# Kernel optimization log

Hardware: AMD Instinct MI355X
Metric: run time of the kernel (lower is better)

Reference implementation:

```python
import jax, jax.numpy as jnp
import numpy as np

B, C, L, H = 4, 512, 2048, 8
D = C // H  # head_dim


def setup_inputs() -> dict:
    key = jax.random.key(0)
    ks = jax.random.split(key, 9)
    s = 1.0 / np.sqrt(C)  # keep logits well-scaled like torch Linear init
    return {
        "x": jax.random.normal(ks[0], (B, C, L), dtype=jnp.float32),
        "Wq": jax.random.normal(ks[1], (C, C), dtype=jnp.float32) * s,
        "bq": jnp.zeros((C,), dtype=jnp.float32),
        "Wk": jax.random.normal(ks[2], (C, C), dtype=jnp.float32) * s,
        "bk": jnp.zeros((C,), dtype=jnp.float32),
        "Wv": jax.random.normal(ks[3], (C, C), dtype=jnp.float32) * s,
        "bv": jnp.zeros((C,), dtype=jnp.float32),
        "Wo": jax.random.normal(ks[4], (C, C), dtype=jnp.float32) * s,
        "bo": jnp.zeros((C,), dtype=jnp.float32),
    }


def reference(x, Wq, bq, Wk, bk, Wv, bv, Wo, bo):
    # x: (B, C, L) -> (B, L, C)
    xp = jnp.transpose(x, (0, 2, 1))
    scale = D ** (-0.5)

    def heads(w, b):
        y = xp @ w.T + b                      # (B, L, C)  torch Linear: x W^T + b
        return y.reshape(B, L, H, D).transpose(0, 2, 1, 3)  # (B, H, L, D)

    q = heads(Wq, bq)
    k = heads(Wk, bk)
    v = heads(Wv, bv)

    attn = jnp.einsum('bhqd,bhkd->bhqk', q, k) * scale  # (B, H, L, L)
    attn = jax.nn.softmax(attn, axis=-1)
    out = jnp.einsum('bhqk,bhkd->bhqd', attn, v)        # (B, H, L, D)
    out = out.transpose(0, 2, 1, 3).reshape(B, L, C)    # (B, L, C)
    out = out @ Wo.T + bo
    return x + jnp.transpose(out, (0, 2, 1))            # residual in (B, C, L)
```

## Files before the change

### kernel.cpp

```cpp
#include <hip/hip_runtime.h>
#include <math.h>

#define B_ 4
#define C_ 512
#define L_ 2048
#define H_ 8
#define D_ 64
#define QSCALE 0.18033688011112042f
#define DEFER_THR 12.0f

typedef __bf16 bf16x8 __attribute__((ext_vector_type(8)));
typedef float f32x4 __attribute__((ext_vector_type(4)));

__device__ __forceinline__ unsigned cvt_pk(float lo, float hi) {
    unsigned r;
    asm("v_cvt_pk_bf16_f32 %0, %1, %2" : "=v"(r) : "v"(lo), "v"(hi));
    return r;
}
__device__ __forceinline__ unsigned short f2bf_hw(float a) {
    unsigned r;
    asm("v_cvt_pk_bf16_f32 %0, %1, %1" : "=v"(r) : "v"(a));
    return (unsigned short)r;
}
__device__ __forceinline__ bf16x8 frag_ld(const unsigned short* p) {
    uint4 v = *reinterpret_cast<const uint4*>(p);
    return __builtin_bit_cast(bf16x8, v);
}
__device__ __forceinline__ float fmax3(float a, float b, float c) {
    return fmaxf(fmaxf(a, b), c);
}
__device__ __forceinline__ void glds16(const void* g, void* l) {
    __builtin_amdgcn_global_load_lds(
        (const __attribute__((address_space(1))) void*)g,
        (__attribute__((address_space(3))) void*)l, 16, 0, 0);
}

__global__ __launch_bounds__(256) void prep(
    const float* __restrict__ x,
    const float* __restrict__ w0, const float* __restrict__ w1,
    const float* __restrict__ w2, const float* __restrict__ w3,
    unsigned short* __restrict__ xt,
    unsigned short* __restrict__ o0, unsigned short* __restrict__ o1,
    unsigned short* __restrict__ o2, unsigned short* __restrict__ o3)
{
    __shared__ float T[64][68];
    const int t = threadIdx.x;

    if (blockIdx.z < B_) {
        const int b  = blockIdx.z;
        const int l0 = blockIdx.x * 64;
        const int c0 = blockIdx.y * 64;
        const float* xb = x + (size_t)b * C_ * L_;
        unsigned short* xtb = xt + (size_t)b * L_ * C_;

        #pragma unroll
        for (int p = 0; p < 4; ++p) {
            const int ci = 16 * p + (t >> 4);
            const int l4 = (t & 15) * 4;
            *reinterpret_cast<float4*>(&T[ci][l4]) =
                *reinterpret_cast<const float4*>(xb + (size_t)(c0 + ci) * L_ + l0 + l4);
        }
        __syncthreads();

        const int lo = t >> 2;
        const int cb = (t & 3) * 16;
        unsigned w[8];
        #pragma unroll
        for (int k = 0; k < 8; ++k)
            w[k] = cvt_pk(T[cb + 2 * k][lo], T[cb + 2 * k + 1][lo]);
        unsigned short* dst = xtb + (size_t)(l0 + lo) * C_ + c0 + cb;
        *reinterpret_cast<uint4*>(dst)     = make_uint4(w[0], w[1], w[2], w[3]);
        *reinterpret_cast<uint4*>(dst + 8) = make_uint4(w[4], w[5], w[6], w[7]);
    } else {
        const int m = blockIdx.z - B_;
        const float* src; unsigned short* dst;
        if      (m == 0) { src = w0; dst = o0; }
        else if (m == 1) { src = w1; dst = o1; }
        else if (m == 2) { src = w2; dst = o2; }
        else             { src = w3; dst = o3; }
        const int flat = blockIdx.x + 32 * blockIdx.y;
        const size_t idx = ((size_t)flat * 256 + t) * 4;
        const float4 v = *reinterpret_cast<const float4*>(src + idx);
        *reinterpret_cast<uint2*>(dst + idx) =
            make_uint2(cvt_pk(v.x, v.y), cvt_pk(v.z, v.w));
    }
}

__global__ __launch_bounds__(256) void qkv_gemm(
    const unsigned short* __restrict__ xt,
    const unsigned short* __restrict__ wq, const unsigned short* __restrict__ wk,
    const unsigned short* __restrict__ wv,
    const float* __restrict__ bq, const float* __restrict__ bk,
    const float* __restrict__ bv,
    unsigned short* __restrict__ qb, unsigned short* __restrict__ kb,
    unsigned short* __restrict__ vb)
{
    __shared__ unsigned short As[2][128][32];
    __shared__ unsigned short Bs[2][128][32];

    const int mode = blockIdx.z >> 2;
    const int b    = blockIdx.z & 3;
    const size_t LC = (size_t)L_ * C_;

    const unsigned short *A, *Bt;
    const float* bias;
    unsigned short* Out;
    float scale = 1.0f;
    int m0, n0, oN, biasN;
    if (mode == 0) {
        A = xt + (size_t)b * LC; Bt = wq; bias = bq; Out = qb + (size_t)b * LC;
        m0 = blockIdx.y * 128; n0 = blockIdx.x * 128; oN = C_; biasN = 1;
        scale = QSCALE;
    } else if (mode == 1) {
        A = xt + (size_t)b * LC; Bt = wk; bias = bk; Out = kb + (size_t)b * LC;
        m0 = blockIdx.y * 128; n0 = blockIdx.x * 128; oN = C_; biasN = 1;
    } else {
        A = wv; Bt = xt + (size_t)b * LC; bias = bv; Out = vb + (size_t)b * LC;
        m0 = blockIdx.x * 128; n0 = blockIdx.y * 128; oN = L_; biasN = 0;
    }
    const int doswz = (mode != 0);

    const int t = threadIdx.x;
    const int lane = t & 63, wid = t >> 6;
    const int wm = (wid >> 1) * 64, wn = (wid & 1) * 64;
    const int q16 = lane & 15, g = lane >> 4;

    const int gr = wid * 32 + (lane >> 2);
    const int gc = (lane & 3) * 8;
    const unsigned short* Ap0 = A  + (size_t)(m0 + gr) * C_ + gc;
    const unsigned short* Ap1 = Ap0 + 16 * C_;
    const unsigned short* Bp0 = Bt + (size_t)(n0 + gr) * C_ + gc;
    const unsigned short* Bp1 = Bp0 + 16 * C_;

    f32x4 zero4 = {0.f, 0.f, 0.f, 0.f};
    f32x4 acc[4][4];
    #pragma unroll
    for (int i = 0; i < 4; ++i)
        #pragma unroll
        for (int j = 0; j < 4; ++j) acc[i][j] = zero4;

    glds16(Ap0, &As[0][wid * 32][0]);      glds16(Ap1, &As[0][wid * 32 + 16][0]);
    glds16(Bp0, &Bs[0][wid * 32][0]);      glds16(Bp1, &Bs[0][wid * 32 + 16][0]);
    __syncthreads();

    #pragma unroll 2
    for (int it = 0; it < 16; ++it) {
        const int cur = it & 1;
        if (it < 15) {
            const int ko = (it + 1) * 32;
            glds16(Ap0 + ko, &As[cur ^ 1][wid * 32][0]);
            glds16(Ap1 + ko, &As[cur ^ 1][wid * 32 + 16][0]);
            glds16(Bp0 + ko, &Bs[cur ^ 1][wid * 32][0]);
            glds16(Bp1 + ko, &Bs[cur ^ 1][wid * 32 + 16][0]);
        }
        bf16x8 af[4], bfr[4];
        #pragma unroll
        for (int i = 0; i < 4; ++i) af[i]  = frag_ld(&As[cur][wm + 16 * i + q16][8 * g]);
        #pragma unroll
        for (int j = 0; j < 4; ++j) bfr[j] = frag_ld(&Bs[cur][wn + 16 * j + q16][8 * g]);
        #pragma unroll
        for (int i = 0; i < 4; ++i)
            #pragma unroll
            for (int j = 0; j < 4; ++j)
                acc[i][j] = __builtin_amdgcn_mfma_f32_16x16x32_bf16(
                    af[i], bfr[j], acc[i][j], 0, 0, 0);
        __syncthreads();
    }

    #pragma unroll
    for (int j = 0; j < 4; ++j) {
        const int n = n0 + wn + 16 * j + q16;
        const float bn = biasN ? bias[n] : 0.f;
        #pragma unroll
        for (int i = 0; i < 4; ++i) {
            #pragma unroll
            for (int r = 0; r < 4; ++r) {
                const int m = m0 + wm + 16 * i + 4 * g + r;
                const float v = acc[i][j][r] + (biasN ? bn : bias[m]);
                const int nn = doswz ? (n ^ ((m & 7) << 3)) : n;
                Out[(size_t)m * oN + nn] = f2bf_hw(v * scale);
            }
        }
    }
}

__global__ __launch_bounds__(256) void gemm_out(
    const unsigned short* __restrict__ A,
    const unsigned short* __restrict__ Bt,
    const float* __restrict__ bias,
    float* __restrict__ Out, const float* __restrict__ resid)
{
    __shared__ unsigned short As[128][40];
    __shared__ unsigned short Bs[128][40];

    const int bz = blockIdx.z;
    const size_t LC = (size_t)L_ * C_;
    Bt    += (size_t)bz * LC;
    Out   += (size_t)bz * LC;
    resid += (size_t)bz * LC;

    const int n0 = blockIdx.x * 128;
    const int m0 = blockIdx.y * 128;
    const int t  = threadIdx.x;
    const int lane = t & 63, wid = t >> 6;
    const int wm = (wid >> 1) * 64, wn = (wid & 1) * 64;
    const int q16 = lane & 15, g = lane >> 4;

    const int srow = t >> 1;
    const int scol = (t & 1) * 16;
    const unsigned short* Ap = A  + (size_t)(m0 + srow) * C_ + scol;
    const unsigned short* Bp = Bt + (size_t)(n0 + srow) * C_ + scol;

    f32x4 zero4 = {0.f, 0.f, 0.f, 0.f};
    f32x4 acc[4][4];
    #pragma unroll
    for (int i = 0; i < 4; ++i)
        #pragma unroll
        for (int j = 0; j < 4; ++j) acc[i][j] = zero4;

    uint4 ar0 = *reinterpret_cast<const uint4*>(Ap);
    uint4 ar1 = *reinterpret_cast<const uint4*>(Ap + 8);
    uint4 br0 = *reinterpret_cast<const uint4*>(Bp);
    uint4 br1 = *reinterpret_cast<const uint4*>(Bp + 8);

    for (int k0 = 0; k0 < C_; k0 += 32) {
        __syncthreads();
        *reinterpret_cast<uint4*>(&As[srow][scol])     = ar0;
        *reinterpret_cast<uint4*>(&As[srow][scol + 8]) = ar1;
        *reinterpret_cast<uint4*>(&Bs[srow][scol])     = br0;
        *reinterpret_cast<uint4*>(&Bs[srow][scol + 8]) = br1;
        __syncthreads();
        if (k0 + 32 < C_) {
            ar0 = *reinterpret_cast<const uint4*>(Ap + k0 + 32);
            ar1 = *reinterpret_cast<const uint4*>(Ap + k0 + 40);
            br0 = *reinterpret_cast<const uint4*>(Bp + k0 + 32);
            br1 = *reinterpret_cast<const uint4*>(Bp + k0 + 40);
        }
        bf16x8 af[4], bfr[4];
        #pragma unroll
        for (int i = 0; i < 4; ++i) af[i]  = frag_ld(&As[wm + 16 * i + q16][8 * g]);
        #pragma unroll
        for (int j = 0; j < 4; ++j) bfr[j] = frag_ld(&Bs[wn + 16 * j + q16][8 * g]);
        #pragma unroll
        for (int i = 0; i < 4; ++i)
            #pragma unroll
            for (int j = 0; j < 4; ++j)
                acc[i][j] = __builtin_amdgcn_mfma_f32_16x16x32_bf16(
                    af[i], bfr[j], acc[i][j], 0, 0, 0);
    }

    #pragma unroll
    for (int j = 0; j < 4; ++j) {
        const int n = n0 + wn + 16 * j + q16;
        #pragma unroll
        for (int i = 0; i < 4; ++i) {
            #pragma unroll
            for (int r = 0; r < 4; ++r) {
                const int m = m0 + wm + 16 * i + 4 * g + r;
                const size_t off = (size_t)m * L_ + n;
                Out[off] = acc[i][j][r] + bias[m] + resid[off];
            }
        }
    }
}

__global__ __launch_bounds__(256) void attn_mfma(
    const unsigned short* __restrict__ Qb,
    const unsigned short* __restrict__ Kb,
    const unsigned short* __restrict__ Vb,
    unsigned short* __restrict__ Ab)
{
    __shared__ unsigned short Ks[2][64][64];
    __shared__ unsigned short Vs[2][64][64];
    __shared__ unsigned short Pw[4][16][64];

    const int q0 = blockIdx.x * 64;
    const int h  = blockIdx.y;
    const int b  = blockIdx.z;
    const int t  = threadIdx.x, lane = t & 63, wid = t >> 6;
    const int q16 = lane & 15, g = lane >> 4;
    const int swz = (q16 & 7) << 3;
    const int h4  = (q16 & 7) << 2;

    const unsigned short* Qg = Qb + (size_t)b * L_ * C_;
    const unsigned short* Kg = Kb + (size_t)b * L_ * C_ + h * D_;
    const unsigned short* Vg = Vb + ((size_t)b * C_ + h * D_) * L_;
    unsigned short* Ag       = Ab + (size_t)b * L_ * C_;

    unsigned* pw = reinterpret_cast<unsigned*>(&Pw[wid][q16][0]);

    bf16x8 qf[2];
    {
        const unsigned short* qp =
            Qg + (size_t)(q0 + 16 * wid + q16) * C_ + h * D_ + 8 * g;
        qf[0] = frag_ld(qp);
        qf[1] = frag_ld(qp + 32);
    }

    const unsigned ow = (q16 == 0) ? 0x3F803F80u : 0u;
    const uint4 ov = make_uint4(ow, ow, ow, ow);
    const bf16x8 onesf = __builtin_bit_cast(bf16x8, ov);

    f32x4 zero4 = {0.f, 0.f, 0.f, 0.f};
    f32x4 oacc[4], lacc = zero4;
    #pragma unroll
    for (int n = 0; n < 4; ++n) oacc[n] = zero4;
    float m_s = -INFINITY;

    const int gr8 = lane >> 3;
    const int gc8 = (lane & 7) * 8;
    const unsigned short* Kp0 = Kg + (size_t)(16 * wid     + gr8) * C_ + gc8;
    const unsigned short* Kp1 = Kg + (size_t)(16 * wid + 8 + gr8) * C_ + gc8;
    const unsigned short* Vp0 = Vg + (size_t)(16 * wid     + gr8) * L_ + gc8;
    const unsigned short* Vp1 = Vg + (size_t)(16 * wid + 8 + gr8) * L_ + gc8;

    glds16(Kp0, &Ks[0][16 * wid][0]);
    glds16(Kp1, &Ks[0][16 * wid + 8][0]);
    glds16(Vp0, &Vs[0][16 * wid][0]);
    glds16(Vp1, &Vs[0][16 * wid + 8][0]);
    __syncthreads();

    #pragma unroll 2
    for (int kt = 0; kt < 32; ++kt) {
        const int cur = kt & 1;
        if (kt < 31) {
            const size_t ko = (size_t)(kt + 1) * 64;
            glds16(Kp0 + ko * C_, &Ks[cur ^ 1][16 * wid][0]);
            glds16(Kp1 + ko * C_, &Ks[cur ^ 1][16 * wid + 8][0]);
            glds16(Vp0 + ko,      &Vs[cur ^ 1][16 * wid][0]);
            glds16(Vp1 + ko,      &Vs[cur ^ 1][16 * wid + 8][0]);
        }

        f32x4 sacc[4];
        #pragma unroll
        for (int f = 0; f < 4; ++f) sacc[f] = zero4;
        #pragma unroll
        for (int s = 0; s < 2; ++s) {
            #pragma unroll
            for (int f = 0; f < 4; ++f) {
                bf16x8 kf = frag_ld(&Ks[cur][16 * f + q16][(32 * s + 8 * g) ^ swz]);
                sacc[f] = __builtin_amdgcn_mfma_f32_16x16x32_bf16(
                    kf, qf[s], sacc[f], 0, 0, 0);
            }
        }

        const float t0 = fmax3(sacc[0][0], sacc[0][1], sacc[0][2]);
        const float t1 = fmax3(sacc[0][3], sacc[1][0], sacc[1][1]);
        const float t2 = fmax3(sacc[1][2], sacc[1][3], sacc[2][0]);
        const float t3 = fmax3(sacc[2][1], sacc[2][2], sacc[2][3]);
        const float t4 = fmax3(sacc[3][0], sacc[3][1], sacc[3][2]);
        float pm = fmaxf(fmax3(t0, t1, t2), fmax3(t3, t4, sacc[3][3]));
        pm = fmaxf(pm, __shfl_xor(pm, 16));
        pm = fmaxf(pm, __shfl_xor(pm, 32));

        if (!__all(pm - m_s <= DEFER_THR)) {
            const float mn   = fmaxf(m_s, pm);
            const float corr = exp2f(m_s - mn);
            m_s = mn;
            #pragma unroll
            for (int r = 0; r < 4; ++r) {
                const float c_o = __shfl(corr, 20 * g + r);
                #pragma unroll
                for (int n = 0; n < 4; ++n) oacc[n][r] *= c_o;
                lacc[r] *= c_o;
            }
        }

        float p[4][4];
        #pragma unroll
        for (int f = 0; f < 4; ++f)
            #pragma unroll
            for (int r = 0; r < 4; ++r) p[f][r] = exp2f(sacc[f][r] - m_s);

        #pragma unroll
        for (int f = 0; f < 4; ++f) {
            uint2 v2;
            v2.x = cvt_pk(p[f][0], p[f][1]);
            v2.y = cvt_pk(p[f][2], p[f][3]);
            *reinterpret_cast<uint2*>(pw + ((8 * f + 2 * g) ^ h4)) = v2;
        }

        #pragma unroll
        for (int s2 = 0; s2 < 2; ++s2) {
            bf16x8 pf = frag_ld(reinterpret_cast<const unsigned short*>(
                pw + ((16 * s2 + 4 * g) ^ h4)));
            #pragma unroll
            for (int n = 0; n < 4; ++n) {
                bf16x8 vf = frag_ld(&Vs[cur][16 * n + q16][(32 * s2 + 8 * g) ^ swz]);
                oacc[n] = __builtin_amdgcn_mfma_f32_16x16x32_bf16(
                    pf, vf, oacc[n], 0, 0, 0);
            }
            lacc = __builtin_amdgcn_mfma_f32_16x16x32_bf16(
                pf, onesf, lacc, 0, 0, 0);
        }

        __syncthreads();
    }

    #pragma unroll
    for (int r = 0; r < 4; ++r) {
        const float l_o = __shfl(lacc[r], lane & 48);
        const float inv = 1.f / l_o;
        const int q = q0 + 16 * wid + 4 * g + r;
        #pragma unroll
        for (int n = 0; n < 4; ++n)
            Ag[(size_t)q * C_ + h * D_ + 16 * n + q16] = f2bf_hw(oacc[n][r] * inv);
    }
}

extern "C" void kernel_launch(void* const* d_in, const int* in_sizes, int n_in,
                              void* d_out, int out_size, void* d_ws, size_t ws_size,
                              hipStream_t stream)
{
    const float* x  = (const float*)d_in[0];
    const float* Wq = (const float*)d_in[1];
    const float* bq = (const float*)d_in[2];
    const float* Wk = (const float*)d_in[3];
    const float* bk = (const float*)d_in[4];
    const float* Wv = (const float*)d_in[5];
    const float* bv = (const float*)d_in[6];
    const float* Wo = (const float*)d_in[7];
    const float* bo = (const float*)d_in[8];
    float* out = (float*)d_out;

    const size_t NB = (size_t)B_ * L_ * C_;
    const size_t NW = (size_t)C_ * C_;
    unsigned short* ws16 = (unsigned short*)d_ws;
    unsigned short* xt  = ws16;
    unsigned short* qb  = xt  + NB;
    unsigned short* kb  = qb  + NB;
    unsigned short* vb  = kb  + NB;
    unsigned short* att = vb  + NB;
    unsigned short* wqb = att + NB;
    unsigned short* wkb = wqb + NW;
    unsigned short* wvb = wkb + NW;
    unsigned short* wob = wvb + NW;

    prep<<<dim3(32, 8, 2 * B_), 256, 0, stream>>>(
        x, Wq, Wk, Wv, Wo, xt, wqb, wkb, wvb, wob);

    qkv_gemm<<<dim3(4, 16, 3 * B_), 256, 0, stream>>>(
        xt, wqb, wkb, wvb, bq, bk, bv, qb, kb, vb);

    attn_mfma<<<dim3(L_ / 64, H_, B_), 256, 0, stream>>>(qb, kb, vb, att);

    gemm_out<<<dim3(16, 4, B_), 256, 0, stream>>>(wob, att, bo, out, x);
}
```

Baseline: 225.1 us.

## Use 32x32 MFMA attention with register P via permlane swap; async double-buffer out GEMM

The attention kernel now uses 32x32x16 MFMA tiles with 128 queries per block, so each block reuses each K/V tile across twice as many queries. It also keeps P in registers, repacking it with v_permlane32_swap instead of round-tripping through LDS. The output GEMM now loads tiles with global-to-LDS direct loads into double-buffered shared memory, replacing register staging and dropping one of the two syncs per k-step. The trade-offs are fewer blocks (512 attention blocks), higher register pressure from the 16-wide accumulators, and unpadded LDS rows in the GEMM that may cause bank conflicts.

```diff
diff --git a/kernel.cpp b/kernel.cpp
--- a/kernel.cpp
+++ b/kernel.cpp
@@ -11,6 +11,7 @@
 
 typedef __bf16 bf16x8 __attribute__((ext_vector_type(8)));
 typedef float f32x4 __attribute__((ext_vector_type(4)));
+typedef float f32x16 __attribute__((ext_vector_type(16)));
 
 __device__ __forceinline__ unsigned cvt_pk(float lo, float hi) {
     unsigned r;
@@ -190,8 +191,8 @@
     const float* __restrict__ bias,
     float* __restrict__ Out, const float* __restrict__ resid)
 {
-    __shared__ unsigned short As[128][40];
-    __shared__ unsigned short Bs[128][40];
+    __shared__ unsigned short As[2][128][32];
+    __shared__ unsigned short Bs[2][128][32];
 
     const int bz = blockIdx.z;
     const size_t LC = (size_t)L_ * C_;
@@ -206,10 +207,12 @@
     const int wm = (wid >> 1) * 64, wn = (wid & 1) * 64;
     const int q16 = lane & 15, g = lane >> 4;
 
-    const int srow = t >> 1;
-    const int scol = (t & 1) * 16;
-    const unsigned short* Ap = A  + (size_t)(m0 + srow) * C_ + scol;
-    const unsigned short* Bp = Bt + (size_t)(n0 + srow) * C_ + scol;
+    const int gr = wid * 32 + (lane >> 2);
+    const int gc = (lane & 3) * 8;
+    const unsigned short* Ap0 = A  + (size_t)(m0 + gr) * C_ + gc;
+    const unsigned short* Ap1 = Ap0 + 16 * C_;
+    const unsigned short* Bp0 = Bt + (size_t)(n0 + gr) * C_ + gc;
+    const unsigned short* Bp1 = Bp0 + 16 * C_;
 
     f32x4 zero4 = {0.f, 0.f, 0.f, 0.f};
     f32x4 acc[4][4];
@@ -218,35 +221,32 @@
         #pragma unroll
         for (int j = 0; j < 4; ++j) acc[i][j] = zero4;
 
-    uint4 ar0 = *reinterpret_cast<const uint4*>(Ap);
-    uint4 ar1 = *reinterpret_cast<const uint4*>(Ap + 8);
-    uint4 br0 = *reinterpret_cast<const uint4*>(Bp);
-    uint4 br1 = *reinterpret_cast<const uint4*>(Bp + 8);
-
-    for (int k0 = 0; k0 < C_; k0 += 32) {
-        __syncthreads();
-        *reinterpret_cast<uint4*>(&As[srow][scol])     = ar0;
-        *reinterpret_cast<uint4*>(&As[srow][scol + 8]) = ar1;
-        *reinterpret_cast<uint4*>(&Bs[srow][scol])     = br0;
-        *reinterpret_cast<uint4*>(&Bs[srow][scol + 8]) = br1;
-        __syncthreads();
-        if (k0 + 32 < C_) {
-            ar0 = *reinterpret_cast<const uint4*>(Ap + k0 + 32);
-            ar1 = *reinterpret_cast<const uint4*>(Ap + k0 + 40);
-            br0 = *reinterpret_cast<const uint4*>(Bp + k0 + 32);
-            br1 = *reinterpret_cast<const uint4*>(Bp + k0 + 40);
+    glds16(Ap0, &As[0][wid * 32][0]);      glds16(Ap1, &As[0][wid * 32 + 16][0]);
+    glds16(Bp0, &Bs[0][wid * 32][0]);      glds16(Bp1, &Bs[0][wid * 32 + 16][0]);
+    __syncthreads();
+
+    #pragma unroll 2
+    for (int it = 0; it < 16; ++it) {
+        const int cur = it & 1;
+        if (it < 15) {
+            const int ko = (it + 1) * 32;
+            glds16(Ap0 + ko, &As[cur ^ 1][wid * 32][0]);
+            glds16(Ap1 + ko, &As[cur ^ 1][wid * 32 + 16][0]);
+            glds16(Bp0 + ko, &Bs[cur ^ 1][wid * 32][0]);
+            glds16(Bp1 + ko, &Bs[cur ^ 1][wid * 32 + 16][0]);
         }
         bf16x8 af[4], bfr[4];
         #pragma unroll
-        for (int i = 0; i < 4; ++i) af[i]  = frag_ld(&As[wm + 16 * i + q16][8 * g]);
-        #pragma unroll
-        for (int j = 0; j < 4; ++j) bfr[j] = frag_ld(&Bs[wn + 16 * j + q16][8 * g]);
+        for (int i = 0; i < 4; ++i) af[i]  = frag_ld(&As[cur][wm + 16 * i + q16][8 * g]);
+        #pragma unroll
+        for (int j = 0; j < 4; ++j) bfr[j] = frag_ld(&Bs[cur][wn + 16 * j + q16][8 * g]);
         #pragma unroll
         for (int i = 0; i < 4; ++i)
             #pragma unroll
             for (int j = 0; j < 4; ++j)
                 acc[i][j] = __builtin_amdgcn_mfma_f32_16x16x32_bf16(
                     af[i], bfr[j], acc[i][j], 0, 0, 0);
+        __syncthreads();
     }
 
     #pragma unroll
@@ -272,47 +272,42 @@
 {
     __shared__ unsigned short Ks[2][64][64];
     __shared__ unsigned short Vs[2][64][64];
-    __shared__ unsigned short Pw[4][16][64];
-
-    const int q0 = blockIdx.x * 64;
+
+    const int q0 = blockIdx.x * 128;
     const int h  = blockIdx.y;
     const int b  = blockIdx.z;
     const int t  = threadIdx.x, lane = t & 63, wid = t >> 6;
-    const int q16 = lane & 15, g = lane >> 4;
-    const int swz = (q16 & 7) << 3;
-    const int h4  = (q16 & 7) << 2;
+    const int q32 = lane & 31, hi = lane >> 5;
+    const int swz = (q32 & 7) << 3;
 
     const unsigned short* Qg = Qb + (size_t)b * L_ * C_;
     const unsigned short* Kg = Kb + (size_t)b * L_ * C_ + h * D_;
     const unsigned short* Vg = Vb + ((size_t)b * C_ + h * D_) * L_;
     unsigned short* Ag       = Ab + (size_t)b * L_ * C_;
 
-    unsigned* pw = reinterpret_cast<unsigned*>(&Pw[wid][q16][0]);
-
-    bf16x8 qf[2];
+    bf16x8 qf[4];
     {
         const unsigned short* qp =
-            Qg + (size_t)(q0 + 16 * wid + q16) * C_ + h * D_ + 8 * g;
-        qf[0] = frag_ld(qp);
-        qf[1] = frag_ld(qp + 32);
-    }
-
-    const unsigned ow = (q16 == 0) ? 0x3F803F80u : 0u;
+            Qg + (size_t)(q0 + 32 * wid + q32) * C_ + h * D_ + 8 * hi;
+        #pragma unroll
+        for (int c = 0; c < 4; ++c) qf[c] = frag_ld(qp + 16 * c);
+    }
+
+    const unsigned ow = (q32 == 0) ? 0x3F803F80u : 0u;
     const uint4 ov = make_uint4(ow, ow, ow, ow);
     const bf16x8 onesf = __builtin_bit_cast(bf16x8, ov);
 
-    f32x4 zero4 = {0.f, 0.f, 0.f, 0.f};
-    f32x4 oacc[4], lacc = zero4;
-    #pragma unroll
-    for (int n = 0; n < 4; ++n) oacc[n] = zero4;
+    f32x16 zero16 = {0.f,0.f,0.f,0.f,0.f,0.f,0.f,0.f,
+                     0.f,0.f,0.f,0.f,0.f,0.f,0.f,0.f};
+    f32x16 oacc0 = zero16, oacc1 = zero16, lacc = zero16;
     float m_s = -INFINITY;
 
     const int gr8 = lane >> 3;
     const int gc8 = (lane & 7) * 8;
-    const unsigned short* Kp0 = Kg + (size_t)(16 * wid     + gr8) * C_ + gc8;
-    const unsigned short* Kp1 = Kg + (size_t)(16 * wid + 8 + gr8) * C_ + gc8;
-    const unsigned short* Vp0 = Vg + (size_t)(16 * wid     + gr8) * L_ + gc8;
-    const unsigned short* Vp1 = Vg + (size_t)(16 * wid + 8 + gr8) * L_ + gc8;
+    const unsigned short* Kp0 = Kg + (size_t)(16 * wid + gr8) * C_ + gc8;
+    const unsigned short* Kp1 = Kp0 + (size_t)8 * C_;
+    const unsigned short* Vp0 = Vg + (size_t)(16 * wid + gr8) * L_ + gc8;
+    const unsigned short* Vp1 = Vp0 + (size_t)8 * L_;
 
     glds16(Kp0, &Ks[0][16 * wid][0]);
     glds16(Kp1, &Ks[0][16 * wid + 8][0]);
@@ -331,26 +326,31 @@
             glds16(Vp1 + ko,      &Vs[cur ^ 1][16 * wid + 8][0]);
         }
 
-        f32x4 sacc[4];
-        #pragma unroll
-        for (int f = 0; f < 4; ++f) sacc[f] = zero4;
-        #pragma unroll
-        for (int s = 0; s < 2; ++s) {
-            #pragma unroll
-            for (int f = 0; f < 4; ++f) {
-                bf16x8 kf = frag_ld(&Ks[cur][16 * f + q16][(32 * s + 8 * g) ^ swz]);
-                sacc[f] = __builtin_amdgcn_mfma_f32_16x16x32_bf16(
-                    kf, qf[s], sacc[f], 0, 0, 0);
-            }
-        }
-
-        const float t0 = fmax3(sacc[0][0], sacc[0][1], sacc[0][2]);
-        const float t1 = fmax3(sacc[0][3], sacc[1][0], sacc[1][1]);
-        const float t2 = fmax3(sacc[1][2], sacc[1][3], sacc[2][0]);
-        const float t3 = fmax3(sacc[2][1], sacc[2][2], sacc[2][3]);
-        const float t4 = fmax3(sacc[3][0], sacc[3][1], sacc[3][2]);
-        float pm = fmaxf(fmax3(t0, t1, t2), fmax3(t3, t4, sacc[3][3]));
-        pm = fmaxf(pm, __shfl_xor(pm, 16));
+        f32x16 s0 = zero16, s1 = zero16;
+        #pragma unroll
+        for (int c = 0; c < 4; ++c) {
+            const int co = (16 * c + 8 * hi) ^ swz;
+            bf16x8 k0 = frag_ld(&Ks[cur][q32][co]);
+            bf16x8 k1 = frag_ld(&Ks[cur][32 + q32][co]);
+            s0 = __builtin_amdgcn_mfma_f32_32x32x16_bf16(k0, qf[c], s0, 0, 0, 0);
+            s1 = __builtin_amdgcn_mfma_f32_32x32x16_bf16(k1, qf[c], s1, 0, 0, 0);
+        }
+
+        const float a0 = fmax3(s0[0], s0[1], s0[2]);
+        const float a1 = fmax3(s0[3], s0[4], s0[5]);
+        const float a2 = fmax3(s0[6], s0[7], s0[8]);
+        const float a3 = fmax3(s0[9], s0[10], s0[11]);
+        const float a4 = fmax3(s0[12], s0[13], s0[14]);
+        const float a5 = fmax3(s0[15], s1[0], s1[1]);
+        const float a6 = fmax3(s1[2], s1[3], s1[4]);
+        const float a7 = fmax3(s1[5], s1[6], s1[7]);
+        const float a8 = fmax3(s1[8], s1[9], s1[10]);
+        const float a9 = fmax3(s1[11], s1[12], s1[13]);
+        const float b0 = fmax3(a0, a1, a2);
+        const float b1 = fmax3(a3, a4, a5);
+        const float b2 = fmax3(a6, a7, a8);
+        const float b3 = fmax3(a9, s1[14], s1[15]);
+        float pm = fmaxf(fmaxf(b0, b1), fmaxf(b2, b3));
         pm = fmaxf(pm, __shfl_xor(pm, 32));
 
         if (!__all(pm - m_s <= DEFER_THR)) {
@@ -358,53 +358,52 @@
             const float corr = exp2f(m_s - mn);
             m_s = mn;
             #pragma unroll
-            for (int r = 0; r < 4; ++r) {
-                const float c_o = __shfl(corr, 20 * g + r);
-                #pragma unroll
-                for (int n = 0; n < 4; ++n) oacc[n][r] *= c_o;
-                lacc[r] *= c_o;
+            for (int r = 0; r < 16; ++r) {
+                const float cr = __shfl(corr, (r & 3) + 8 * (r >> 2) + 4 * hi);
+                oacc0[r] *= cr; oacc1[r] *= cr; lacc[r] *= cr;
             }
         }
 
-        float p[4][4];
-        #pragma unroll
-        for (int f = 0; f < 4; ++f)
-            #pragma unroll
-            for (int r = 0; r < 4; ++r) p[f][r] = exp2f(sacc[f][r] - m_s);
-
-        #pragma unroll
-        for (int f = 0; f < 4; ++f) {
-            uint2 v2;
-            v2.x = cvt_pk(p[f][0], p[f][1]);
-            v2.y = cvt_pk(p[f][2], p[f][3]);
-            *reinterpret_cast<uint2*>(pw + ((8 * f + 2 * g) ^ h4)) = v2;
-        }
-
-        #pragma unroll
-        for (int s2 = 0; s2 < 2; ++s2) {
-            bf16x8 pf = frag_ld(reinterpret_cast<const unsigned short*>(
-                pw + ((16 * s2 + 4 * g) ^ h4)));
-            #pragma unroll
-            for (int n = 0; n < 4; ++n) {
-                bf16x8 vf = frag_ld(&Vs[cur][16 * n + q16][(32 * s2 + 8 * g) ^ swz]);
-                oacc[n] = __builtin_amdgcn_mfma_f32_16x16x32_bf16(
-                    pf, vf, oacc[n], 0, 0, 0);
-            }
-            lacc = __builtin_amdgcn_mfma_f32_16x16x32_bf16(
-                pf, onesf, lacc, 0, 0, 0);
+        float p0[16], p1[16];
+        #pragma unroll
+        for (int r = 0; r < 16; ++r) {
+            p0[r] = exp2f(s0[r] - m_s);
+            p1[r] = exp2f(s1[r] - m_s);
+        }
+
+        #pragma unroll
+        for (int ks = 0; ks < 4; ++ks) {
+            const int rb = 8 * (ks & 1);
+            #define PPX(i) ((ks < 2) ? p0[(i)] : p1[(i)])
+            unsigned wa = cvt_pk(PPX(rb + 0), PPX(rb + 1));
+            unsigned wb = cvt_pk(PPX(rb + 2), PPX(rb + 3));
+            unsigned wc = cvt_pk(PPX(rb + 4), PPX(rb + 5));
+            unsigned wd = cvt_pk(PPX(rb + 6), PPX(rb + 7));
+            #undef PPX
+            asm volatile("v_permlane32_swap_b32 %0, %1" : "+v"(wa), "+v"(wc));
+            asm volatile("v_permlane32_swap_b32 %0, %1" : "+v"(wb), "+v"(wd));
+            const uint4 pv = make_uint4(wa, wb, wc, wd);
+            const bf16x8 paf = __builtin_bit_cast(bf16x8, pv);
+
+            const int co = (16 * ks + 8 * hi) ^ swz;
+            bf16x8 v0 = frag_ld(&Vs[cur][q32][co]);
+            bf16x8 v1 = frag_ld(&Vs[cur][32 + q32][co]);
+            oacc0 = __builtin_amdgcn_mfma_f32_32x32x16_bf16(paf, v0, oacc0, 0, 0, 0);
+            oacc1 = __builtin_amdgcn_mfma_f32_32x32x16_bf16(paf, v1, oacc1, 0, 0, 0);
+            lacc  = __builtin_amdgcn_mfma_f32_32x32x16_bf16(paf, onesf, lacc, 0, 0, 0);
         }
 
         __syncthreads();
     }
 
     #pragma unroll
-    for (int r = 0; r < 4; ++r) {
-        const float l_o = __shfl(lacc[r], lane & 48);
-        const float inv = 1.f / l_o;
-        const int q = q0 + 16 * wid + 4 * g + r;
-        #pragma unroll
-        for (int n = 0; n < 4; ++n)
-            Ag[(size_t)q * C_ + h * D_ + 16 * n + q16] = f2bf_hw(oacc[n][r] * inv);
+    for (int r = 0; r < 16; ++r) {
+        const float lv  = __shfl(lacc[r], hi << 5);
+        const float inv = 1.f / lv;
+        const int q = q0 + 32 * wid + (r & 3) + 8 * (r >> 2) + 4 * hi;
+        unsigned short* op = Ag + (size_t)q * C_ + h * D_ + q32;
+        op[0]  = f2bf_hw(oacc0[r] * inv);
+        op[32] = f2bf_hw(oacc1[r] * inv);
     }
 }
 
@@ -442,7 +441,7 @@
     qkv_gemm<<<dim3(4, 16, 3 * B_), 256, 0, stream>>>(
         xt, wqb, wkb, wvb, bq, bk, bv, qb, kb, vb);
 
-    attn_mfma<<<dim3(L_ / 64, H_, B_), 256, 0, stream>>>(qb, kb, vb, att);
+    attn_mfma<<<dim3(L_ / 128, H_, B_), 256, 0, stream>>>(qb, kb, vb, att);
 
     gemm_out<<<dim3(16, 4, B_), 256, 0, stream>>>(wob, att, bo, out, x);
 }
```

New measurement: 208.6 us. 7.4% less time.
